# Kernel optimization log

Measured on AMD Instinct MI355X. Metric: run time of the kernel, lower is better.

The kernel has to match this reference:

```python
import jax, jax.numpy as jnp
import numpy as np

N = 100000
E = 3200000
D = 128


def _sage(x, src, dst, Wl, bl, Wr, n):
    # PyG SAGEConv default: mean-aggregate neighbor features, then
    # out = lin_l(mean_agg) + lin_r(x); bias only in lin_l.
    msg_sum = jax.ops.segment_sum(x[src], dst, num_segments=n)          # [N, D]
    deg = jax.ops.segment_sum(jnp.ones((src.shape[0],), x.dtype), dst, num_segments=n)
    mean = msg_sum / jnp.maximum(deg, 1.0)[:, None]
    return mean @ Wl.T + bl + x @ Wr.T


def setup_inputs() -> dict:
    key = jax.random.key(0)
    ks = jax.random.split(key, 8)
    s = 1.0 / np.sqrt(D)
    inp = {
        "x": jax.random.normal(ks[0], (N, D), dtype=jnp.float32),
        "edge_index": jax.random.randint(ks[1], (2, E), 0, N, dtype=jnp.int64),
    }
    names = ["W1l", "W1r", "W2l", "W2r", "W3l", "W3r"]
    for i, nm in enumerate(names):
        inp[nm] = jax.random.uniform(ks[2 + i % 6], (D, D), jnp.float32, -s, s)
    for nm, kk in zip(["b1", "b2", "b3"], jax.random.split(ks[7], 3)):
        inp[nm] = jax.random.uniform(kk, (D,), jnp.float32, -s, s)
    return inp


def reference(x, edge_index, W1l, W1r, W2l, W2r, W3l, W3r, b1, b2, b3):
    src, dst = edge_index[0], edge_index[1]
    n = x.shape[0]
    h = _sage(x, src, dst, W1l, b1, W1r, n)
    h = jax.nn.relu(h)  # dropout treated as identity (eval mode) for determinism
    h = _sage(h, src, dst, W2l, b2, W2r, n)
    h = jax.nn.relu(h)
    h = _sage(h, src, dst, W3l, b3, W3r, n)
    return h
```

## Files before the change

### kernel.cpp

```cpp
#include <hip/hip_runtime.h>
#include <hip/hip_fp16.h>

#define FD 128
#define BSHIFT 9
#define BNODES 512
#define CAP 20480
#define SBLK 1024

typedef _Float16 half8 __attribute__((ext_vector_type(8)));
typedef float floatx4 __attribute__((ext_vector_type(4)));

__global__ __launch_bounds__(256) void to_f16_kernel(const float4* __restrict__ in,
                                                     __half2* __restrict__ out, int n4) {
    int i = blockIdx.x * 256 + threadIdx.x;
    if (i < n4) {
        float4 v = in[i];
        out[2 * i + 0] = __floats2half2_rn(v.x, v.y);
        out[2 * i + 1] = __floats2half2_rn(v.z, v.w);
    }
}

__global__ __launch_bounds__(256) void pack_w3_kernel(const float* __restrict__ W1l,
                                                      const float* __restrict__ W1r,
                                                      const float* __restrict__ W2l,
                                                      const float* __restrict__ W2r,
                                                      const float* __restrict__ W3l,
                                                      const float* __restrict__ W3r,
                                                      half8* __restrict__ out) {
    int t = blockIdx.x * 256 + threadIdx.x;
    int layer = t >> 12;
    int li = t & 4095;
    const float* Wl = (layer == 0) ? W1l : (layer == 1) ? W2l : W3l;
    const float* Wr = (layer == 0) ? W1r : (layer == 1) ? W2r : W3r;
    int lane = li & 63;
    int kt = (li >> 6) & 7;
    int nt = li >> 9;
    int n = nt * 16 + (lane & 15);
    int kq = kt * 32 + ((lane >> 4) & 3) * 8;
    half8 f;
#pragma unroll
    for (int j = 0; j < 8; ++j) {
        int k = kq + j;
        float v = (k < 128) ? Wl[n * 128 + k] : Wr[n * 128 + (k - 128)];
        f[j] = (_Float16)v;
    }
    out[t] = f;
}

__global__ __launch_bounds__(256) void scatter_kernel(const int* __restrict__ src,
                                                      const int* __restrict__ dst,
                                                      int* __restrict__ cursor,
                                                      int2* __restrict__ sorted, int E) {
    __shared__ int cnt[256];
    __shared__ int base[256];
    int t = threadIdx.x;
    cnt[t] = 0;
    __syncthreads();
    int chunk = (E + SBLK - 1) / SBLK;
    int s0 = blockIdx.x * chunk;
    int s1 = s0 + chunk; if (s1 > E) s1 = E;
    for (int e = s0 + t; e < s1; e += 256)
        atomicAdd(&cnt[dst[e] >> BSHIFT], 1);
    __syncthreads();
    int c = cnt[t];
    if (c > 0) base[t] = atomicAdd(&cursor[t], c);
    cnt[t] = 0;
    __syncthreads();
    for (int e = s0 + t; e < s1; e += 256) {
        int d = dst[e];
        int b = d >> BSHIFT;
        int p = base[b] + atomicAdd(&cnt[b], 1);
        if (p < CAP) sorted[(size_t)b * CAP + p] = make_int2(src[e], d);
    }
}

__global__ __launch_bounds__(256) void bucket_build(const int2* __restrict__ sorted,
                                                    const int* __restrict__ cursor,
                                                    int* __restrict__ row_ptr,
                                                    int* __restrict__ deg,
                                                    float* __restrict__ rdeg,
                                                    int* __restrict__ csr, int N) {
    __shared__ int dl[BNODES];
    __shared__ int ps[256];
    int b = blockIdx.x;
    int nbase = b << BSHIFT;
    int t = threadIdx.x;
    int cnt = cursor[b]; if (cnt > CAP) cnt = CAP;
    dl[t] = 0; dl[t + 256] = 0;
    __syncthreads();
    const int2* se = sorted + (size_t)b * CAP;
    for (int e = t; e < cnt; e += 256)
        atomicAdd(&dl[se[e].y - nbase], 1);
    __syncthreads();
    int a0 = dl[2 * t], a1 = dl[2 * t + 1];
    ps[t] = a0 + a1;
    __syncthreads();
    for (int off = 1; off < 256; off <<= 1) {
        int v = (t >= off) ? ps[t - off] : 0;
        __syncthreads();
        ps[t] += v;
        __syncthreads();
    }
    int pre = ps[t] - a0 - a1;
    int cb = b * CAP;
    int n0 = nbase + 2 * t, n1 = n0 + 1;
    if (n0 < N) {
        row_ptr[n0] = cb + pre;
        deg[n0] = a0;
        rdeg[n0] = 1.0f / (float)(a0 > 1 ? a0 : 1);
    }
    if (n1 < N) {
        row_ptr[n1] = cb + pre + a0;
        deg[n1] = a1;
        rdeg[n1] = 1.0f / (float)(a1 > 1 ? a1 : 1);
    }
    dl[2 * t] = pre;
    dl[2 * t + 1] = pre + a0;
    __syncthreads();
    for (int e = t; e < cnt; e += 256) {
        int2 ed = se[e];
        int p = atomicAdd(&dl[ed.y - nbase], 1);
        csr[cb + p] = ed.x;
    }
}

__global__ __launch_bounds__(256) void agg_kernel(const __half* __restrict__ h,
                                                  const int* __restrict__ row_ptr,
                                                  const int* __restrict__ deg,
                                                  const float* __restrict__ rdeg,
                                                  const int* __restrict__ csr,
                                                  __half* __restrict__ out, int n) {
    int node = (blockIdx.x * 256 + threadIdx.x) >> 6;
    int lane = threadIdx.x & 63;
    if (node >= n) return;
    int g = lane >> 4;
    int l16 = lane & 15;
    int start = row_ptr[node];
    int d = deg[node];
    float acc[8];
#pragma unroll
    for (int j = 0; j < 8; ++j) acc[j] = 0.f;

    int i = 0;
    for (; i + 16 <= d; i += 16) {
        int s0 = csr[start + i + 0 + g];
        int s1 = csr[start + i + 4 + g];
        int s2 = csr[start + i + 8 + g];
        int s3 = csr[start + i + 12 + g];
        half8 v0 = *(const half8*)(h + (size_t)s0 * FD + l16 * 8);
        half8 v1 = *(const half8*)(h + (size_t)s1 * FD + l16 * 8);
        half8 v2 = *(const half8*)(h + (size_t)s2 * FD + l16 * 8);
        half8 v3 = *(const half8*)(h + (size_t)s3 * FD + l16 * 8);
#pragma unroll
        for (int j = 0; j < 8; ++j) acc[j] += (float)v0[j];
#pragma unroll
        for (int j = 0; j < 8; ++j) acc[j] += (float)v1[j];
#pragma unroll
        for (int j = 0; j < 8; ++j) acc[j] += (float)v2[j];
#pragma unroll
        for (int j = 0; j < 8; ++j) acc[j] += (float)v3[j];
    }
    for (; i + 4 <= d; i += 4) {
        int s = csr[start + i + g];
        half8 v = *(const half8*)(h + (size_t)s * FD + l16 * 8);
#pragma unroll
        for (int j = 0; j < 8; ++j) acc[j] += (float)v[j];
    }
    if (i + g < d) {
        int s = csr[start + i + g];
        half8 v = *(const half8*)(h + (size_t)s * FD + l16 * 8);
#pragma unroll
        for (int j = 0; j < 8; ++j) acc[j] += (float)v[j];
    }

#pragma unroll
    for (int j = 0; j < 8; ++j) {
        acc[j] += __shfl_xor(acc[j], 16, 64);
        acc[j] += __shfl_xor(acc[j], 32, 64);
    }

    if (g == 0) {
        float r = rdeg[node];
        half8 o;
#pragma unroll
        for (int j = 0; j < 8; ++j) o[j] = (_Float16)(acc[j] * r);
        *(half8*)(out + (size_t)node * FD + l16 * 8) = o;
    }
}

template <int OUT_FP32>
__global__ __launch_bounds__(256) void gemm_mfma(const __half* __restrict__ A,
                                                 const __half* __restrict__ H,
                                                 const half8* __restrict__ Wfrag,
                                                 const float* __restrict__ bias,
                                                 void* outp, int n, int do_relu) {
    int tid = threadIdx.x;
    int wave = tid >> 6;
    int lane = tid & 63;
    int quad = (lane >> 4) & 3;
    int l16 = lane & 15;
    long tilebase = (long)blockIdx.x * 128;
    long r0 = tilebase + wave * 32 + l16;
    long r1 = r0 + 16;
    long ra = (r0 < n) ? r0 : (n - 1);
    long rb = (r1 < n) ? r1 : (n - 1);

    floatx4 acc[2][8];
#pragma unroll
    for (int m = 0; m < 2; ++m)
#pragma unroll
        for (int nt = 0; nt < 8; ++nt) acc[m][nt] = (floatx4){0.f, 0.f, 0.f, 0.f};

#pragma unroll
    for (int kt = 0; kt < 8; ++kt) {
        const __half* src = (kt < 4) ? A : H;
        int koff = (kt & 3) * 32 + quad * 8;
        half8 a0 = *(const half8*)(src + (size_t)ra * FD + koff);
        half8 a1 = *(const half8*)(src + (size_t)rb * FD + koff);
#pragma unroll
        for (int nt = 0; nt < 8; ++nt) {
            half8 b = Wfrag[(size_t)(nt * 8 + kt) * 64 + lane];
            acc[0][nt] = __builtin_amdgcn_mfma_f32_16x16x32_f16(a0, b, acc[0][nt], 0, 0, 0);
            acc[1][nt] = __builtin_amdgcn_mfma_f32_16x16x32_f16(a1, b, acc[1][nt], 0, 0, 0);
        }
    }

#pragma unroll
    for (int m = 0; m < 2; ++m) {
#pragma unroll
        for (int nt = 0; nt < 8; ++nt) {
            int col = nt * 16 + l16;
            float bv = bias[col];
#pragma unroll
            for (int r = 0; r < 4; ++r) {
                long row = tilebase + wave * 32 + m * 16 + quad * 4 + r;
                if (row < n) {
                    float v = acc[m][nt][r] + bv;
                    if (do_relu) v = v > 0.f ? v : 0.f;
                    if (OUT_FP32)
                        ((float*)outp)[row * FD + col] = v;
                    else
                        ((__half*)outp)[row * FD + col] = __float2half_rn(v);
                }
            }
        }
    }
}

extern "C" void kernel_launch(void* const* d_in, const int* in_sizes, int n_in,
                              void* d_out, int out_size, void* d_ws, size_t ws_size,
                              hipStream_t stream) {
    const float* x   = (const float*)d_in[0];
    const int*   ei  = (const int*)d_in[1];
    const float* W1l = (const float*)d_in[2];
    const float* W1r = (const float*)d_in[3];
    const float* W2l = (const float*)d_in[4];
    const float* W2r = (const float*)d_in[5];
    const float* W3l = (const float*)d_in[6];
    const float* W3r = (const float*)d_in[7];
    const float* b1  = (const float*)d_in[8];
    const float* b2  = (const float*)d_in[9];
    const float* b3  = (const float*)d_in[10];
    float* out = (float*)d_out;

    int N = in_sizes[0] / FD;
    int E = in_sizes[1] / 2;
    const int* src = ei;
    const int* dst = ei + E;
    int B = (N + BNODES - 1) >> BSHIFT;

    char* ws = (char*)d_ws;
    size_t off = 0;
    auto alloc = [&](size_t bytes) -> void* {
        void* p = ws + off;
        off += (bytes + 255) & ~(size_t)255;
        return p;
    };
    int*    deg     = (int*)alloc((size_t)N * 4);
    int*    row_ptr = (int*)alloc((size_t)N * 4);
    float*  rdeg    = (float*)alloc((size_t)N * 4);
    int*    cursor  = (int*)alloc(256 * 4);
    int*    csr     = (int*)alloc((size_t)B * CAP * 4);
    __half* xb      = (__half*)alloc((size_t)N * FD * 2);
    __half* h1      = (__half*)alloc((size_t)N * FD * 2);
    __half* h2      = (__half*)alloc((size_t)N * FD * 2);
    __half* aggB    = (__half*)alloc((size_t)N * FD * 2);
    half8*  wf      = (half8*)alloc((size_t)3 * 4096 * 16);
    int2*   sorted  = (int2*)alloc((size_t)B * CAP * 8);

    int n4 = N * FD / 4;
    to_f16_kernel<<<(n4 + 255) / 256, 256, 0, stream>>>((const float4*)x, (__half2*)xb, n4);
    pack_w3_kernel<<<48, 256, 0, stream>>>(W1l, W1r, W2l, W2r, W3l, W3r, wf);
    hipMemsetAsync(cursor, 0, 256 * 4, stream);
    scatter_kernel<<<SBLK, 256, 0, stream>>>(src, dst, cursor, sorted, E);
    bucket_build<<<B, 256, 0, stream>>>(sorted, cursor, row_ptr, deg, rdeg, csr, N);

    int aggGrid  = (N + 3) / 4;
    int gemmGrid = (N + 127) / 128;

    agg_kernel<<<aggGrid, 256, 0, stream>>>(xb, row_ptr, deg, rdeg, csr, aggB, N);
    gemm_mfma<0><<<gemmGrid, 256, 0, stream>>>(aggB, xb, wf, b1, h1, N, 1);
    agg_kernel<<<aggGrid, 256, 0, stream>>>(h1, row_ptr, deg, rdeg, csr, aggB, N);
    gemm_mfma<0><<<gemmGrid, 256, 0, stream>>>(aggB, h1, wf + 4096, b2, h2, N, 1);
    agg_kernel<<<aggGrid, 256, 0, stream>>>(h2, row_ptr, deg, rdeg, csr, aggB, N);
    gemm_mfma<1><<<gemmGrid, 256, 0, stream>>>(aggB, h2, wf + 8192, b3, out, N, 0);
}
```

Measured before the change: 706.6 us.

## Fuse all stages into one persistent kernel with global barriers

Replaces the chain of separate launches (f16 convert, weight pack, scatter, bucket build, three agg+gemm pairs) with a single persistent kernel of 1024 blocks that steps through the phases, separated by atomic-counter grid barriers. Agg and gemm phases become grid-stride loops. It also packs each sorted edge into one 32-bit int (local dst in the high bits, src in the low 17) instead of an int2, halving that intermediate's traffic. The aim is to remove launch gaps and tail effects. The risks are deadlock if not all 1024 blocks are co-resident, a spin-timeout break that could silently corrupt results, and lower occupancy for the memory-bound gather.

Result: slower. 1.886 ms (+167.0%).

```diff
diff --git a/kernel.cpp b/kernel.cpp
--- a/kernel.cpp
+++ b/kernel.cpp
@@ -5,33 +5,66 @@
 #define BSHIFT 9
 #define BNODES 512
 #define CAP 20480
-#define SBLK 1024
+#define GRID 1024
+#define NT 256
 
 typedef _Float16 half8 __attribute__((ext_vector_type(8)));
 typedef float floatx4 __attribute__((ext_vector_type(4)));
 
-__global__ __launch_bounds__(256) void to_f16_kernel(const float4* __restrict__ in,
-                                                     __half2* __restrict__ out, int n4) {
-    int i = blockIdx.x * 256 + threadIdx.x;
-    if (i < n4) {
+struct Params {
+    const float* x;
+    const int* src;
+    const int* dst;
+    const float* W1l; const float* W1r;
+    const float* W2l; const float* W2r;
+    const float* W3l; const float* W3r;
+    const float* b1; const float* b2; const float* b3;
+    float* out;
+    int* cursor; int* sorted; int* row_ptr; int* deg; float* rdeg; int* csr;
+    int* bar;
+    __half* xb; __half* h1; __half* h2; __half* aggB;
+    half8* wf;
+    int N, E, B;
+};
+
+union SharedU {
+    struct { int cnt[256]; int base[256]; } sc;
+    struct { int dl[BNODES]; int ps[256]; } bb;
+};
+
+__device__ __forceinline__ void gbar(int* cnt, int nblk) {
+    __syncthreads();
+    if (threadIdx.x == 0) {
+        __threadfence();
+        atomicAdd(cnt, 1);
+        int spins = 0;
+        while (__hip_atomic_load(cnt, __ATOMIC_RELAXED, __HIP_MEMORY_SCOPE_AGENT) < nblk) {
+            __builtin_amdgcn_s_sleep(2);
+            if (++spins > (1 << 24)) break;
+        }
+        __threadfence();
+    }
+    __syncthreads();
+}
+
+__device__ void phase_tof16(const Params& p, int gid, int total) {
+    int n4 = p.N * FD / 4;
+    const float4* in = (const float4*)p.x;
+    __half2* out = (__half2*)p.xb;
+    for (int i = gid; i < n4; i += total) {
         float4 v = in[i];
         out[2 * i + 0] = __floats2half2_rn(v.x, v.y);
         out[2 * i + 1] = __floats2half2_rn(v.z, v.w);
     }
 }
 
-__global__ __launch_bounds__(256) void pack_w3_kernel(const float* __restrict__ W1l,
-                                                      const float* __restrict__ W1r,
-                                                      const float* __restrict__ W2l,
-                                                      const float* __restrict__ W2r,
-                                                      const float* __restrict__ W3l,
-                                                      const float* __restrict__ W3r,
-                                                      half8* __restrict__ out) {
-    int t = blockIdx.x * 256 + threadIdx.x;
+__device__ void phase_pack(const Params& p, int gid) {
+    if (gid >= 12288) return;
+    int t = gid;
     int layer = t >> 12;
     int li = t & 4095;
-    const float* Wl = (layer == 0) ? W1l : (layer == 1) ? W2l : W3l;
-    const float* Wr = (layer == 0) ? W1r : (layer == 1) ? W2r : W3r;
+    const float* Wl = (layer == 0) ? p.W1l : (layer == 1) ? p.W2l : p.W3l;
+    const float* Wr = (layer == 0) ? p.W1r : (layer == 1) ? p.W2r : p.W3r;
     int lane = li & 63;
     int kt = (li >> 6) & 7;
     int nt = li >> 9;
@@ -44,53 +77,41 @@
         float v = (k < 128) ? Wl[n * 128 + k] : Wr[n * 128 + (k - 128)];
         f[j] = (_Float16)v;
     }
-    out[t] = f;
-}
-
-__global__ __launch_bounds__(256) void scatter_kernel(const int* __restrict__ src,
-                                                      const int* __restrict__ dst,
-                                                      int* __restrict__ cursor,
-                                                      int2* __restrict__ sorted, int E) {
-    __shared__ int cnt[256];
-    __shared__ int base[256];
+    p.wf[t] = f;
+}
+
+__device__ void phase_scatter(const Params& p, int* cnt, int* base) {
     int t = threadIdx.x;
     cnt[t] = 0;
     __syncthreads();
-    int chunk = (E + SBLK - 1) / SBLK;
+    int chunk = (p.E + GRID - 1) / GRID;
     int s0 = blockIdx.x * chunk;
-    int s1 = s0 + chunk; if (s1 > E) s1 = E;
-    for (int e = s0 + t; e < s1; e += 256)
-        atomicAdd(&cnt[dst[e] >> BSHIFT], 1);
+    int s1 = s0 + chunk; if (s1 > p.E) s1 = p.E;
+    for (int e = s0 + t; e < s1; e += NT)
+        atomicAdd(&cnt[p.dst[e] >> BSHIFT], 1);
     __syncthreads();
     int c = cnt[t];
-    if (c > 0) base[t] = atomicAdd(&cursor[t], c);
+    if (c > 0) base[t] = atomicAdd(&p.cursor[t], c);
     cnt[t] = 0;
     __syncthreads();
-    for (int e = s0 + t; e < s1; e += 256) {
-        int d = dst[e];
+    for (int e = s0 + t; e < s1; e += NT) {
+        int d = p.dst[e];
         int b = d >> BSHIFT;
-        int p = base[b] + atomicAdd(&cnt[b], 1);
-        if (p < CAP) sorted[(size_t)b * CAP + p] = make_int2(src[e], d);
-    }
-}
-
-__global__ __launch_bounds__(256) void bucket_build(const int2* __restrict__ sorted,
-                                                    const int* __restrict__ cursor,
-                                                    int* __restrict__ row_ptr,
-                                                    int* __restrict__ deg,
-                                                    float* __restrict__ rdeg,
-                                                    int* __restrict__ csr, int N) {
-    __shared__ int dl[BNODES];
-    __shared__ int ps[256];
+        int pp = base[b] + atomicAdd(&cnt[b], 1);
+        if (pp < CAP) p.sorted[(size_t)b * CAP + pp] = ((d & (BNODES - 1)) << 17) | p.src[e];
+    }
+}
+
+__device__ void phase_build(const Params& p, int* dl, int* ps) {
     int b = blockIdx.x;
     int nbase = b << BSHIFT;
     int t = threadIdx.x;
-    int cnt = cursor[b]; if (cnt > CAP) cnt = CAP;
+    int cnt = p.cursor[b]; if (cnt > CAP) cnt = CAP;
     dl[t] = 0; dl[t + 256] = 0;
     __syncthreads();
-    const int2* se = sorted + (size_t)b * CAP;
-    for (int e = t; e < cnt; e += 256)
-        atomicAdd(&dl[se[e].y - nbase], 1);
+    const int* se = p.sorted + (size_t)b * CAP;
+    for (int e = t; e < cnt; e += NT)
+        atomicAdd(&dl[((unsigned)se[e]) >> 17], 1);
     __syncthreads();
     int a0 = dl[2 * t], a1 = dl[2 * t + 1];
     ps[t] = a0 + a1;
@@ -104,204 +125,211 @@
     int pre = ps[t] - a0 - a1;
     int cb = b * CAP;
     int n0 = nbase + 2 * t, n1 = n0 + 1;
-    if (n0 < N) {
-        row_ptr[n0] = cb + pre;
-        deg[n0] = a0;
-        rdeg[n0] = 1.0f / (float)(a0 > 1 ? a0 : 1);
-    }
-    if (n1 < N) {
-        row_ptr[n1] = cb + pre + a0;
-        deg[n1] = a1;
-        rdeg[n1] = 1.0f / (float)(a1 > 1 ? a1 : 1);
+    if (n0 < p.N) {
+        p.row_ptr[n0] = cb + pre;
+        p.deg[n0] = a0;
+        p.rdeg[n0] = 1.0f / (float)(a0 > 1 ? a0 : 1);
+    }
+    if (n1 < p.N) {
+        p.row_ptr[n1] = cb + pre + a0;
+        p.deg[n1] = a1;
+        p.rdeg[n1] = 1.0f / (float)(a1 > 1 ? a1 : 1);
     }
     dl[2 * t] = pre;
     dl[2 * t + 1] = pre + a0;
     __syncthreads();
-    for (int e = t; e < cnt; e += 256) {
-        int2 ed = se[e];
-        int p = atomicAdd(&dl[ed.y - nbase], 1);
-        csr[cb + p] = ed.x;
-    }
-}
-
-__global__ __launch_bounds__(256) void agg_kernel(const __half* __restrict__ h,
-                                                  const int* __restrict__ row_ptr,
-                                                  const int* __restrict__ deg,
-                                                  const float* __restrict__ rdeg,
-                                                  const int* __restrict__ csr,
-                                                  __half* __restrict__ out, int n) {
-    int node = (blockIdx.x * 256 + threadIdx.x) >> 6;
+    for (int e = t; e < cnt; e += NT) {
+        int v = se[e];
+        int pp = atomicAdd(&dl[((unsigned)v) >> 17], 1);
+        p.csr[cb + pp] = v & 0x1FFFF;
+    }
+}
+
+__device__ void phase_agg(const Params& p, const __half* h, __half* out) {
+    int wave = threadIdx.x >> 6;
     int lane = threadIdx.x & 63;
-    if (node >= n) return;
     int g = lane >> 4;
     int l16 = lane & 15;
-    int start = row_ptr[node];
-    int d = deg[node];
-    float acc[8];
-#pragma unroll
-    for (int j = 0; j < 8; ++j) acc[j] = 0.f;
-
-    int i = 0;
-    for (; i + 16 <= d; i += 16) {
-        int s0 = csr[start + i + 0 + g];
-        int s1 = csr[start + i + 4 + g];
-        int s2 = csr[start + i + 8 + g];
-        int s3 = csr[start + i + 12 + g];
-        half8 v0 = *(const half8*)(h + (size_t)s0 * FD + l16 * 8);
-        half8 v1 = *(const half8*)(h + (size_t)s1 * FD + l16 * 8);
-        half8 v2 = *(const half8*)(h + (size_t)s2 * FD + l16 * 8);
-        half8 v3 = *(const half8*)(h + (size_t)s3 * FD + l16 * 8);
-#pragma unroll
-        for (int j = 0; j < 8; ++j) acc[j] += (float)v0[j];
-#pragma unroll
-        for (int j = 0; j < 8; ++j) acc[j] += (float)v1[j];
-#pragma unroll
-        for (int j = 0; j < 8; ++j) acc[j] += (float)v2[j];
-#pragma unroll
-        for (int j = 0; j < 8; ++j) acc[j] += (float)v3[j];
-    }
-    for (; i + 4 <= d; i += 4) {
-        int s = csr[start + i + g];
-        half8 v = *(const half8*)(h + (size_t)s * FD + l16 * 8);
-#pragma unroll
-        for (int j = 0; j < 8; ++j) acc[j] += (float)v[j];
-    }
-    if (i + g < d) {
-        int s = csr[start + i + g];
-        half8 v = *(const half8*)(h + (size_t)s * FD + l16 * 8);
-#pragma unroll
-        for (int j = 0; j < 8; ++j) acc[j] += (float)v[j];
-    }
-
-#pragma unroll
-    for (int j = 0; j < 8; ++j) {
-        acc[j] += __shfl_xor(acc[j], 16, 64);
-        acc[j] += __shfl_xor(acc[j], 32, 64);
-    }
-
-    if (g == 0) {
-        float r = rdeg[node];
-        half8 o;
-#pragma unroll
-        for (int j = 0; j < 8; ++j) o[j] = (_Float16)(acc[j] * r);
-        *(half8*)(out + (size_t)node * FD + l16 * 8) = o;
+    for (int node = blockIdx.x * 4 + wave; node < p.N; node += GRID * 4) {
+        int start = p.row_ptr[node];
+        int d = p.deg[node];
+        float acc[8];
+#pragma unroll
+        for (int j = 0; j < 8; ++j) acc[j] = 0.f;
+        int i = 0;
+        for (; i + 16 <= d; i += 16) {
+            int s0 = p.csr[start + i + 0 + g];
+            int s1 = p.csr[start + i + 4 + g];
+            int s2 = p.csr[start + i + 8 + g];
+            int s3 = p.csr[start + i + 12 + g];
+            half8 v0 = *(const half8*)(h + (size_t)s0 * FD + l16 * 8);
+            half8 v1 = *(const half8*)(h + (size_t)s1 * FD + l16 * 8);
+            half8 v2 = *(const half8*)(h + (size_t)s2 * FD + l16 * 8);
+            half8 v3 = *(const half8*)(h + (size_t)s3 * FD + l16 * 8);
+#pragma unroll
+            for (int j = 0; j < 8; ++j) acc[j] += (float)v0[j];
+#pragma unroll
+            for (int j = 0; j < 8; ++j) acc[j] += (float)v1[j];
+#pragma unroll
+            for (int j = 0; j < 8; ++j) acc[j] += (float)v2[j];
+#pragma unroll
+            for (int j = 0; j < 8; ++j) acc[j] += (float)v3[j];
+        }
+        for (; i + 4 <= d; i += 4) {
+            int s = p.csr[start + i + g];
+            half8 v = *(const half8*)(h + (size_t)s * FD + l16 * 8);
+#pragma unroll
+            for (int j = 0; j < 8; ++j) acc[j] += (float)v[j];
+        }
+        if (i + g < d) {
+            int s = p.csr[start + i + g];
+            half8 v = *(const half8*)(h + (size_t)s * FD + l16 * 8);
+#pragma unroll
+            for (int j = 0; j < 8; ++j) acc[j] += (float)v[j];
+        }
+#pragma unroll
+        for (int j = 0; j < 8; ++j) {
+            acc[j] += __shfl_xor(acc[j], 16, 64);
+            acc[j] += __shfl_xor(acc[j], 32, 64);
+        }
+        if (g == 0) {
+            float r = p.rdeg[node];
+            half8 o;
+#pragma unroll
+            for (int j = 0; j < 8; ++j) o[j] = (_Float16)(acc[j] * r);
+            *(half8*)(out + (size_t)node * FD + l16 * 8) = o;
+        }
     }
 }
 
 template <int OUT_FP32>
-__global__ __launch_bounds__(256) void gemm_mfma(const __half* __restrict__ A,
-                                                 const __half* __restrict__ H,
-                                                 const half8* __restrict__ Wfrag,
-                                                 const float* __restrict__ bias,
-                                                 void* outp, int n, int do_relu) {
+__device__ void phase_gemm(const __half* A, const __half* H, const half8* Wfrag,
+                           const float* bias, void* outp, int n, int do_relu) {
     int tid = threadIdx.x;
     int wave = tid >> 6;
     int lane = tid & 63;
     int quad = (lane >> 4) & 3;
     int l16 = lane & 15;
-    long tilebase = (long)blockIdx.x * 128;
-    long r0 = tilebase + wave * 32 + l16;
-    long r1 = r0 + 16;
-    long ra = (r0 < n) ? r0 : (n - 1);
-    long rb = (r1 < n) ? r1 : (n - 1);
-
-    floatx4 acc[2][8];
-#pragma unroll
-    for (int m = 0; m < 2; ++m)
-#pragma unroll
-        for (int nt = 0; nt < 8; ++nt) acc[m][nt] = (floatx4){0.f, 0.f, 0.f, 0.f};
-
-#pragma unroll
-    for (int kt = 0; kt < 8; ++kt) {
-        const __half* src = (kt < 4) ? A : H;
-        int koff = (kt & 3) * 32 + quad * 8;
-        half8 a0 = *(const half8*)(src + (size_t)ra * FD + koff);
-        half8 a1 = *(const half8*)(src + (size_t)rb * FD + koff);
-#pragma unroll
-        for (int nt = 0; nt < 8; ++nt) {
-            half8 b = Wfrag[(size_t)(nt * 8 + kt) * 64 + lane];
-            acc[0][nt] = __builtin_amdgcn_mfma_f32_16x16x32_f16(a0, b, acc[0][nt], 0, 0, 0);
-            acc[1][nt] = __builtin_amdgcn_mfma_f32_16x16x32_f16(a1, b, acc[1][nt], 0, 0, 0);
-        }
-    }
-
-#pragma unroll
-    for (int m = 0; m < 2; ++m) {
-#pragma unroll
-        for (int nt = 0; nt < 8; ++nt) {
-            int col = nt * 16 + l16;
-            float bv = bias[col];
-#pragma unroll
-            for (int r = 0; r < 4; ++r) {
-                long row = tilebase + wave * 32 + m * 16 + quad * 4 + r;
-                if (row < n) {
-                    float v = acc[m][nt][r] + bv;
-                    if (do_relu) v = v > 0.f ? v : 0.f;
-                    if (OUT_FP32)
-                        ((float*)outp)[row * FD + col] = v;
-                    else
-                        ((__half*)outp)[row * FD + col] = __float2half_rn(v);
+    int ntiles = (n + 127) / 128;
+    for (int tile = blockIdx.x; tile < ntiles; tile += GRID) {
+        long tilebase = (long)tile * 128;
+        long r0 = tilebase + wave * 32 + l16;
+        long r1 = r0 + 16;
+        long ra = (r0 < n) ? r0 : (n - 1);
+        long rb = (r1 < n) ? r1 : (n - 1);
+
+        floatx4 acc[2][8];
+#pragma unroll
+        for (int m = 0; m < 2; ++m)
+#pragma unroll
+            for (int nt = 0; nt < 8; ++nt) acc[m][nt] = (floatx4){0.f, 0.f, 0.f, 0.f};
+
+#pragma unroll
+        for (int kt = 0; kt < 8; ++kt) {
+            const __half* srcp = (kt < 4) ? A : H;
+            int koff = (kt & 3) * 32 + quad * 8;
+            half8 a0 = *(const half8*)(srcp + (size_t)ra * FD + koff);
+            half8 a1 = *(const half8*)(srcp + (size_t)rb * FD + koff);
+#pragma unroll
+            for (int nt = 0; nt < 8; ++nt) {
+                half8 b = Wfrag[(size_t)(nt * 8 + kt) * 64 + lane];
+                acc[0][nt] = __builtin_amdgcn_mfma_f32_16x16x32_f16(a0, b, acc[0][nt], 0, 0, 0);
+                acc[1][nt] = __builtin_amdgcn_mfma_f32_16x16x32_f16(a1, b, acc[1][nt], 0, 0, 0);
+            }
+        }
+
+#pragma unroll
+        for (int m = 0; m < 2; ++m) {
+#pragma unroll
+            for (int nt = 0; nt < 8; ++nt) {
+                int col = nt * 16 + l16;
+                float bv = bias[col];
+#pragma unroll
+                for (int r = 0; r < 4; ++r) {
+                    long row = tilebase + wave * 32 + m * 16 + quad * 4 + r;
+                    if (row < n) {
+                        float v = acc[m][nt][r] + bv;
+                        if (do_relu) v = v > 0.f ? v : 0.f;
+                        if (OUT_FP32)
+                            ((float*)outp)[row * FD + col] = v;
+                        else
+                            ((__half*)outp)[row * FD + col] = __float2half_rn(v);
+                    }
                 }
             }
         }
     }
+}
+
+__global__ __launch_bounds__(256, 4) void fused_all(Params p) {
+    __shared__ SharedU sh;
+    int gid = blockIdx.x * NT + threadIdx.x;
+    int total = GRID * NT;
+
+    phase_tof16(p, gid, total);
+    phase_pack(p, gid);
+    if (gid < 256) p.cursor[gid] = 0;
+    gbar(p.bar + 0, GRID);
+    phase_scatter(p, sh.sc.cnt, sh.sc.base);
+    gbar(p.bar + 1, GRID);
+    if (blockIdx.x < (unsigned)p.B) phase_build(p, sh.bb.dl, sh.bb.ps);
+    gbar(p.bar + 2, GRID);
+    phase_agg(p, p.xb, p.aggB);
+    gbar(p.bar + 3, GRID);
+    phase_gemm<0>(p.aggB, p.xb, p.wf, p.b1, p.h1, p.N, 1);
+    gbar(p.bar + 4, GRID);
+    phase_agg(p, p.h1, p.aggB);
+    gbar(p.bar + 5, GRID);
+    phase_gemm<0>(p.aggB, p.h1, p.wf + 4096, p.b2, p.h2, p.N, 1);
+    gbar(p.bar + 6, GRID);
+    phase_agg(p, p.h2, p.aggB);
+    gbar(p.bar + 7, GRID);
+    phase_gemm<1>(p.aggB, p.h2, p.wf + 8192, p.b3, p.out, p.N, 0);
 }
 
 extern "C" void kernel_launch(void* const* d_in, const int* in_sizes, int n_in,
                               void* d_out, int out_size, void* d_ws, size_t ws_size,
                               hipStream_t stream) {
-    const float* x   = (const float*)d_in[0];
-    const int*   ei  = (const int*)d_in[1];
-    const float* W1l = (const float*)d_in[2];
-    const float* W1r = (const float*)d_in[3];
-    const float* W2l = (const float*)d_in[4];
-    const float* W2r = (const float*)d_in[5];
-    const float* W3l = (const float*)d_in[6];
-    const float* W3r = (const float*)d_in[7];
-    const float* b1  = (const float*)d_in[8];
-    const float* b2  = (const float*)d_in[9];
-    const float* b3  = (const float*)d_in[10];
-    float* out = (float*)d_out;
-
-    int N = in_sizes[0] / FD;
-    int E = in_sizes[1] / 2;
-    const int* src = ei;
-    const int* dst = ei + E;
-    int B = (N + BNODES - 1) >> BSHIFT;
+    Params p;
+    p.x   = (const float*)d_in[0];
+    const int* ei = (const int*)d_in[1];
+    p.W1l = (const float*)d_in[2];
+    p.W1r = (const float*)d_in[3];
+    p.W2l = (const float*)d_in[4];
+    p.W2r = (const float*)d_in[5];
+    p.W3l = (const float*)d_in[6];
+    p.W3r = (const float*)d_in[7];
+    p.b1  = (const float*)d_in[8];
+    p.b2  = (const float*)d_in[9];
+    p.b3  = (const float*)d_in[10];
+    p.out = (float*)d_out;
+
+    p.N = in_sizes[0] / FD;
+    p.E = in_sizes[1] / 2;
+    p.src = ei;
+    p.dst = ei + p.E;
+    p.B = (p.N + BNODES - 1) >> BSHIFT;
 
     char* ws = (char*)d_ws;
     size_t off = 0;
     auto alloc = [&](size_t bytes) -> void* {
-        void* p = ws + off;
+        void* ptr = ws + off;
         off += (bytes + 255) & ~(size_t)255;
-        return p;
+        return ptr;
     };
-    int*    deg     = (int*)alloc((size_t)N * 4);
-    int*    row_ptr = (int*)alloc((size_t)N * 4);
-    float*  rdeg    = (float*)alloc((size_t)N * 4);
-    int*    cursor  = (int*)alloc(256 * 4);
-    int*    csr     = (int*)alloc((size_t)B * CAP * 4);
-    __half* xb      = (__half*)alloc((size_t)N * FD * 2);
-    __half* h1      = (__half*)alloc((size_t)N * FD * 2);
-    __half* h2      = (__half*)alloc((size_t)N * FD * 2);
-    __half* aggB    = (__half*)alloc((size_t)N * FD * 2);
-    half8*  wf      = (half8*)alloc((size_t)3 * 4096 * 16);
-    int2*   sorted  = (int2*)alloc((size_t)B * CAP * 8);
-
-    int n4 = N * FD / 4;
-    to_f16_kernel<<<(n4 + 255) / 256, 256, 0, stream>>>((const float4*)x, (__half2*)xb, n4);
-    pack_w3_kernel<<<48, 256, 0, stream>>>(W1l, W1r, W2l, W2r, W3l, W3r, wf);
-    hipMemsetAsync(cursor, 0, 256 * 4, stream);
-    scatter_kernel<<<SBLK, 256, 0, stream>>>(src, dst, cursor, sorted, E);
-    bucket_build<<<B, 256, 0, stream>>>(sorted, cursor, row_ptr, deg, rdeg, csr, N);
-
-    int aggGrid  = (N + 3) / 4;
-    int gemmGrid = (N + 127) / 128;
-
-    agg_kernel<<<aggGrid, 256, 0, stream>>>(xb, row_ptr, deg, rdeg, csr, aggB, N);
-    gemm_mfma<0><<<gemmGrid, 256, 0, stream>>>(aggB, xb, wf, b1, h1, N, 1);
-    agg_kernel<<<aggGrid, 256, 0, stream>>>(h1, row_ptr, deg, rdeg, csr, aggB, N);
-    gemm_mfma<0><<<gemmGrid, 256, 0, stream>>>(aggB, h1, wf + 4096, b2, h2, N, 1);
-    agg_kernel<<<aggGrid, 256, 0, stream>>>(h2, row_ptr, deg, rdeg, csr, aggB, N);
-    gemm_mfma<1><<<gemmGrid, 256, 0, stream>>>(aggB, h2, wf + 8192, b3, out, N, 0);
-}
+    p.deg     = (int*)alloc((size_t)p.N * 4);
+    p.row_ptr = (int*)alloc((size_t)p.N * 4);
+    p.rdeg    = (float*)alloc((size_t)p.N * 4);
+    p.cursor  = (int*)alloc(256 * 4);
+    p.bar     = (int*)alloc(64 * 4);
+    p.csr     = (int*)alloc((size_t)p.B * CAP * 4);
+    p.xb      = (__half*)alloc((size_t)p.N * FD * 2);
+    p.h1      = (__half*)alloc((size_t)p.N * FD * 2);
+    p.h2      = (__half*)alloc((size_t)p.N * FD * 2);
+    p.aggB    = (__half*)alloc((size_t)p.N * FD * 2);
+    p.wf      = (half8*)alloc((size_t)3 * 4096 * 16);
+    p.sorted  = (int*)alloc((size_t)p.B * CAP * 4);
+
+    hipMemsetAsync(p.bar, 0, 64 * 4, stream);
+    fused_all<<<GRID, NT, 0, stream>>>(p);
+}
```
